# Optimization experiments

Measured on AMD Instinct MI355X. Metric: run time of the kernel, lower is better.

The kernel has to match this reference:

```python
import jax, jax.numpy as jnp
import numpy as np

B, S, D, H = 8, 2048, 1024, 8
HD = D // H


def _linear_params(key, d_in, d_out):
    kw, kb = jax.random.split(key)
    w = jax.random.normal(kw, (d_out, d_in), jnp.float32) * 0.02
    b = jax.random.normal(kb, (d_out,), jnp.float32) * 0.02
    return w, b


def setup_inputs() -> dict:
    key = jax.random.key(0)
    ks = jax.random.split(key, 16)
    inp = {}
    inp['input_seq'] = jax.random.normal(ks[0], (B, S, D), jnp.float32)
    inp['output_seq'] = jax.random.normal(ks[1], (B, S, D), jnp.float32)
    # PositionalEncoding parameter: sin(arange(D) / 10000 ** (arange(D)/D))
    ar = jnp.arange(D, dtype=jnp.float32)
    inp['pe'] = jnp.sin(ar / 10000.0 ** (ar / D))
    names = ['enc_wq enc_bq', 'enc_wk enc_bk', 'enc_wv enc_bv',
             'enc_w1 enc_b1', 'enc_w2 enc_b2',
             'dec_s_wq dec_s_bq', 'dec_s_wk dec_s_bk', 'dec_s_wv dec_s_bv',
             'dec_c_wq dec_c_bq', 'dec_c_wk dec_c_bk', 'dec_c_wv dec_c_bv',
             'dec_w1 dec_b1', 'dec_w2 dec_b2', 'fc_w fc_b']
    for i, pair in enumerate(names):
        wn, bn = pair.split()
        w, b = _linear_params(ks[2 + i], D, D)
        inp[wn], inp[bn] = w, b
    return inp


def _mha(q_in, k_in, wq, bq, wk, bk, wv, bv):
    # Faithful to source: head split WITHOUT transpose -> per-position 8x8 head mixing.
    q = (q_in @ wq.T + bq).reshape(q_in.shape[0], q_in.shape[1], H, HD)
    k = (k_in @ wk.T + bk).reshape(k_in.shape[0], k_in.shape[1], H, HD)
    v = (k_in @ wv.T + bv).reshape(k_in.shape[0], k_in.shape[1], H, HD)
    scores = jnp.einsum('bsih,bsjh->bsij', q, k) / jnp.sqrt(jnp.float32(HD))
    w = jax.nn.softmax(scores, axis=-1)  # dropout before softmax is identity at eval
    out = jnp.einsum('bsij,bsjh->bsih', w, v)
    return out.reshape(q_in.shape[0], q_in.shape[1], -1)


def reference(input_seq, output_seq, pe,
              enc_wq, enc_bq, enc_wk, enc_bk, enc_wv, enc_bv,
              enc_w1, enc_b1, enc_w2, enc_b2,
              dec_s_wq, dec_s_bq, dec_s_wk, dec_s_bk, dec_s_wv, dec_s_bv,
              dec_c_wq, dec_c_bq, dec_c_wk, dec_c_bk, dec_c_wv, dec_c_bv,
              dec_w1, dec_b1, dec_w2, dec_b2, fc_w, fc_b):
    x = input_seq + pe  # additive positional encoding
    # encoder layer
    a = _mha(x, x, enc_wq, enc_bq, enc_wk, enc_bk, enc_wv, enc_bv)
    enc_out = jax.nn.relu(a @ enc_w1.T + enc_b1) @ enc_w2.T + enc_b2
    # decoder layer (training branch: output_seq given)
    sa = _mha(output_seq, output_seq, dec_s_wq, dec_s_bq, dec_s_wk, dec_s_bk, dec_s_wv, dec_s_bv)
    ca = _mha(sa, enc_out, dec_c_wq, dec_c_bq, dec_c_wk, dec_c_bk, dec_c_wv, dec_c_bv)
    dec_out = jax.nn.relu(ca @ dec_w1.T + dec_b1) @ dec_w2.T + dec_b2
    return dec_out @ fc_w.T + fc_b
```

## Files before the change

### kernel.cpp

```cpp
#include <hip/hip_runtime.h>
#include <stdint.h>


#define TOKENS 16384
#define DMODEL 1024

typedef unsigned short ushort_t;
typedef __attribute__((ext_vector_type(8))) short short8;
typedef __attribute__((ext_vector_type(4))) float floatx4;

__device__ __forceinline__ float b2f(ushort_t u) {
  union { uint32_t i; float f; } v; v.i = ((uint32_t)u) << 16; return v.f;
}
__device__ __forceinline__ ushort_t f2b(float f) {
  union { float f; uint32_t i; } v; v.f = f;
  uint32_t r = v.i + 0x7fffu + ((v.i >> 16) & 1u);
  return (ushort_t)(r >> 16);
}

__device__ __forceinline__ void pack8(const float* __restrict__ g, ushort_t* dst) {
  float4 x = *(const float4*)g;
  float4 y = *(const float4*)(g + 4);
  ushort_t o[8] = {f2b(x.x), f2b(x.y), f2b(x.z), f2b(x.w),
                   f2b(y.x), f2b(y.y), f2b(y.z), f2b(y.w)};
  *(uint4*)dst = *(uint4*)o;
}

#define GLD16(g, l)                                                          \
  __builtin_amdgcn_global_load_lds(                                          \
      (const __attribute__((address_space(1))) void*)(g),                    \
      (__attribute__((address_space(3))) void*)(l), 16, 0, 0)

struct ConvArgs {
  const float* src[14];
  ushort_t* dst[14];
};

__global__ __launch_bounds__(256) void conv_w_kernel(ConvArgs a) {
  const int w = blockIdx.y;
  const int idx = (blockIdx.x * 256 + threadIdx.x) * 8;
  pack8(a.src[w] + idx, a.dst[w] + idx);
}

__global__ __launch_bounds__(256) void conv_x_kernel(
    const float* __restrict__ src, ushort_t* __restrict__ dst) {
  const int idx = (blockIdx.x * 256 + threadIdx.x) * 8;
  pack8(src + idx, dst + idx);
}

__global__ __launch_bounds__(256) void add_pe_kernel(
    const float* __restrict__ in, const float* __restrict__ pe,
    ushort_t* __restrict__ out) {
  int idx = (blockIdx.x * 256 + threadIdx.x) * 8;
  int d = idx & (DMODEL - 1);
  float4 a0 = *(const float4*)(in + idx);
  float4 a1 = *(const float4*)(in + idx + 4);
  float4 p0 = *(const float4*)(pe + d);
  float4 p1 = *(const float4*)(pe + d + 4);
  ushort_t o[8] = {f2b(a0.x + p0.x), f2b(a0.y + p0.y), f2b(a0.z + p0.z), f2b(a0.w + p0.w),
                   f2b(a1.x + p1.x), f2b(a1.y + p1.y), f2b(a1.z + p1.z), f2b(a1.w + p1.w)};
  *(uint4*)(out + idx) = *(uint4*)o;
}

template <int D, int MH>
__device__ __forceinline__ void load_a(const ushort_t* sA, int aoff, int cs0,
                                       int cs1, short8 (&af)[4][2]) {
  const ushort_t* p = sA + D * 16384 + MH * 8192 + aoff;
#pragma unroll
  for (int i = 0; i < 4; i++) {
    af[i][0] = *(const short8*)&p[i * 1024 + cs0];
    af[i][1] = *(const short8*)&p[i * 1024 + cs1];
  }
}

template <int D, int NH>
__device__ __forceinline__ void load_b(const ushort_t* sB, int boff, int cs0,
                                       int cs1, short8 (&bf)[2][2]) {
  const ushort_t* p = sB + D * 16384 + NH * 8192 + boff;
#pragma unroll
  for (int j = 0; j < 2; j++) {
    bf[j][0] = *(const short8*)&p[j * 1024 + cs0];
    bf[j][1] = *(const short8*)&p[j * 1024 + cs1];
  }
}

template <int Q>
__device__ __forceinline__ void mfma_q(floatx4 (&acc)[4][4][2],
                                       const short8 (&af)[4][2],
                                       const short8 (&bf)[2][2]) {
  __builtin_amdgcn_s_setprio(1);
#pragma unroll
  for (int i = 0; i < 4; i++)
#pragma unroll
    for (int j = 0; j < 2; j++) {
      acc[Q][i][j] = __builtin_amdgcn_mfma_f32_16x16x32_bf16(
          af[i][0], bf[j][0], acc[Q][i][j], 0, 0, 0);
      acc[Q][i][j] = __builtin_amdgcn_mfma_f32_16x16x32_bf16(
          af[i][1], bf[j][1], acc[Q][i][j], 0, 0, 0);
    }
  __builtin_amdgcn_s_setprio(0);
}

#define BARSB                                                                \
  do {                                                                       \
    __builtin_amdgcn_s_barrier();                                            \
    __builtin_amdgcn_sched_barrier(0);                                       \
  } while (0)

#define STAGE_A(h, tk, d)                                                    \
  do {                                                                       \
    GLD16(gA + (size_t)((h) * 131072 + (tk) * 64),                           \
          sA + (d) * 16384 + (h) * 8192 + lo);                               \
    GLD16(gA + (size_t)((h) * 131072 + 65536 + (tk) * 64),                   \
          sA + (d) * 16384 + (h) * 8192 + 4096 + lo);                        \
  } while (0)
#define STAGE_B(h, tk, d)                                                    \
  do {                                                                       \
    GLD16(gB + (size_t)((h) * 131072 + (tk) * 64),                           \
          sB + (d) * 16384 + (h) * 8192 + lo);                               \
    GLD16(gB + (size_t)((h) * 131072 + 65536 + (tk) * 64),                   \
          sB + (d) * 16384 + (h) * 8192 + 4096 + lo);                        \
  } while (0)

#define GROUP(tt, dd)                                                        \
  do {                                                                       \
    load_a<dd, 0>(sA, aoff, cs0, cs1, af);                                   \
    load_b<dd, 0>(sB, boff, cs0, cs1, bf);                                   \
    if ((tt) + 1 < NT) {                                                     \
      STAGE_B(0, (tt) + 1, dd ^ 1);                                          \
      STAGE_A(1, (tt) + 1, dd ^ 1);                                          \
    }                                                                        \
    BARSB;                                                                   \
    mfma_q<0>(acc, af, bf);                                                  \
    BARSB;                                                                   \
    load_b<dd, 1>(sB, boff, cs0, cs1, bf);                                   \
    BARSB;                                                                   \
    mfma_q<1>(acc, af, bf);                                                  \
    BARSB;                                                                   \
    load_a<dd, 1>(sA, aoff, cs0, cs1, af);                                   \
    if ((tt) + 2 < NT) STAGE_A(0, (tt) + 2, dd);                             \
    BARSB;                                                                   \
    mfma_q<3>(acc, af, bf);                                                  \
    BARSB;                                                                   \
    load_b<dd, 0>(sB, boff, cs0, cs1, bf);                                   \
    if ((tt) + 2 < NT) STAGE_B(1, (tt) + 2, dd);                             \
    BARSB;                                                                   \
    mfma_q<2>(acc, af, bf);                                                  \
    if ((tt) + 2 < NT) {                                                     \
      asm volatile("s_waitcnt vmcnt(4)");                                    \
    } else {                                                                 \
      asm volatile("s_waitcnt vmcnt(0)");                                    \
    }                                                                        \
    BARSB;                                                                   \
  } while (0)

template <bool RELU, bool OUT32>
__global__ __launch_bounds__(512, 2) void gemm_bt(
    const ushort_t* __restrict__ A, const ushort_t* __restrict__ W,
    const float* __restrict__ bias, void* __restrict__ Cp) {
  constexpr int K = 1024, N = 1024, NT = 16;
  extern __shared__ ushort_t smem[];
  ushort_t* sA = smem;
  ushort_t* sB = smem + 32768;

  const int tid = threadIdx.x;
  const int lane = tid & 63;
  const int wid = tid >> 6;

  const int orig = blockIdx.x;
  const int swz = (orig & 7) * 32 + (orig >> 3);
  const int m0 = (swz >> 2) * 256;
  const int n0 = (swz & 3) * 256;

  const int qm = (wid >> 2) * 64;
  const int qn = (wid & 3) * 32;
  const int lr = lane & 15;
  const int lq = lane >> 4;
  const int xr = lane & 7;
  const int cs0 = (lq ^ xr) * 8;
  const int cs1 = ((4 + lq) ^ xr) * 8;
  const int aoff = (qm + lr) * 64;
  const int boff = (qn + lr) * 64;

  const int rl = tid >> 3;
  const int j8 = tid & 7;
  const int co = (j8 ^ (rl & 7)) * 8;
  const int lo = tid * 8;
  const ushort_t* gA = A + (size_t)(m0 + rl) * K + co;
  const ushort_t* gB = W + (size_t)(n0 + rl) * K + co;

  floatx4 acc[4][4][2] = {};
  short8 af[4][2], bf[2][2];

  STAGE_A(0, 0, 0);
  STAGE_B(1, 0, 0);
  STAGE_B(0, 0, 0);
  STAGE_A(1, 0, 0);
  STAGE_A(0, 1, 1);
  STAGE_B(1, 1, 1);
  asm volatile("s_waitcnt vmcnt(4)");
  BARSB;

#pragma unroll 1
  for (int t = 0; t < NT; t += 2) {
    GROUP(t, 0);
    GROUP(t + 1, 1);
  }

  const int rbase = lq * 4;

  if constexpr (OUT32) {
    float* sCf = (float*)smem;
#pragma unroll
    for (int p = 0; p < 4; p++) {
      if ((qm >> 6) == (p & 1)) {
#pragma unroll
        for (int Nh = 0; Nh < 2; Nh++)
#pragma unroll
          for (int j = 0; j < 2; j++) {
            const int col = Nh * 128 + qn + j * 16 + lr;
            const float bv = bias[n0 + col];
#pragma unroll
            for (int i = 0; i < 4; i++)
#pragma unroll
              for (int r = 0; r < 4; r++) {
                float v = acc[(p >> 1) * 2 + Nh][i][j][r] + bv;
                if (RELU) v = fmaxf(v, 0.0f);
                sCf[(i * 16 + rbase + r) * 260 + col] = v;
              }
          }
      }
      __syncthreads();
#pragma unroll
      for (int u = 0; u < 8; u++) {
        const int lin = u * 512 + tid;
        const int row = lin >> 6;
        const int c4 = (lin & 63) * 4;
        *(float4*)((float*)Cp + (size_t)(m0 + p * 64 + row) * N + n0 + c4) =
            *(const float4*)&sCf[row * 260 + c4];
      }
      __syncthreads();
    }
    return;
  }

  ushort_t* sC = smem;
#pragma unroll
  for (int p = 0; p < 2; p++) {
#pragma unroll
    for (int Nh = 0; Nh < 2; Nh++)
#pragma unroll
      for (int j = 0; j < 2; j++) {
        const int col = Nh * 128 + qn + j * 16 + lr;
        const float bv = bias[n0 + col];
#pragma unroll
        for (int i = 0; i < 4; i++)
#pragma unroll
          for (int r = 0; r < 4; r++) {
            float v = acc[p * 2 + Nh][i][j][r] + bv;
            if (RELU) v = fmaxf(v, 0.0f);
            sC[(qm + i * 16 + rbase + r) * 264 + col] = f2b(v);
          }
      }
    __syncthreads();
#pragma unroll
    for (int u = 0; u < 8; u++) {
      const int lin = u * 512 + tid;
      const int row = lin >> 5;
      const int c8 = (lin & 31) * 8;
      *(uint4*)((ushort_t*)Cp + (size_t)(m0 + p * 128 + row) * N + n0 + c8) =
          *(const uint4*)&sC[row * 264 + c8];
    }
    __syncthreads();
  }
}

__global__ __launch_bounds__(256) void attn_kernel(
    const ushort_t* Q, const ushort_t* Kp, const ushort_t* Vp, ushort_t* O) {
  __shared__ __align__(16) ushort_t sq[4][1024];
  __shared__ __align__(16) ushort_t sk[4][1024];
  __shared__ __align__(16) ushort_t sv[4][1024];
  __shared__ float sp[4][64];

  const int t = threadIdx.x;
  const int w = t >> 6;
  const int lane = t & 63;
  const size_t base = ((size_t)blockIdx.x * 4 + w) * 1024;

  ((uint4*)sq[w])[lane] = ((const uint4*)(Q + base))[lane];
  ((uint4*)sq[w])[lane + 64] = ((const uint4*)(Q + base))[lane + 64];
  ((uint4*)sk[w])[lane] = ((const uint4*)(Kp + base))[lane];
  ((uint4*)sk[w])[lane + 64] = ((const uint4*)(Kp + base))[lane + 64];
  ((uint4*)sv[w])[lane] = ((const uint4*)(Vp + base))[lane];
  ((uint4*)sv[w])[lane + 64] = ((const uint4*)(Vp + base))[lane + 64];
  __syncthreads();

  {
    const int i = lane >> 3, j = lane & 7;
    const ushort_t* qr = &sq[w][i * 128];
    const ushort_t* kr = &sk[w][j * 128];
    float s = 0.0f;
#pragma unroll 16
    for (int h = 0; h < 128; h++) s += b2f(qr[h]) * b2f(kr[h]);
    s *= 0.08838834764831845f;
    float m = s;
#pragma unroll
    for (int off = 1; off < 8; off <<= 1) m = fmaxf(m, __shfl_xor(m, off, 64));
    float e = __expf(s - m);
    float sum = e;
#pragma unroll
    for (int off = 1; off < 8; off <<= 1) sum += __shfl_xor(sum, off, 64);
    sp[w][lane] = e / sum;
  }
  __syncthreads();

  {
    const int i = lane >> 3;
    const int hb = (lane & 7) * 16;
    float p[8];
#pragma unroll
    for (int jj = 0; jj < 8; jj++) p[jj] = sp[w][i * 8 + jj];
    float o[16];
#pragma unroll
    for (int h = 0; h < 16; h++) {
      float acc = 0.0f;
#pragma unroll
      for (int jj = 0; jj < 8; jj++) acc += p[jj] * b2f(sv[w][jj * 128 + hb + h]);
      o[h] = acc;
    }
    uint32_t packed[8];
#pragma unroll
    for (int u = 0; u < 8; u++)
      packed[u] = (uint32_t)f2b(o[2 * u]) | ((uint32_t)f2b(o[2 * u + 1]) << 16);
    uint4* dst = (uint4*)(O + base + i * 128 + hb);
    dst[0] = *(uint4*)&packed[0];
    dst[1] = *(uint4*)&packed[4];
  }
}

extern "C" void kernel_launch(void* const* d_in, const int* in_sizes, int n_in,
                              void* d_out, int out_size, void* d_ws, size_t ws_size,
                              hipStream_t stream) {
  const float* input_seq = (const float*)d_in[0];
  const float* output_seq = (const float*)d_in[1];
  const float* pe = (const float*)d_in[2];
  const float* wsrc[14] = {
      (const float*)d_in[3],  (const float*)d_in[5],  (const float*)d_in[7],
      (const float*)d_in[9],  (const float*)d_in[11], (const float*)d_in[13],
      (const float*)d_in[15], (const float*)d_in[17], (const float*)d_in[19],
      (const float*)d_in[21], (const float*)d_in[23], (const float*)d_in[25],
      (const float*)d_in[27], (const float*)d_in[29]};
  const float* enc_bq = (const float*)d_in[4];
  const float* enc_bk = (const float*)d_in[6];
  const float* enc_bv = (const float*)d_in[8];
  const float* enc_b1 = (const float*)d_in[10];
  const float* enc_b2 = (const float*)d_in[12];
  const float* dsq_b = (const float*)d_in[14];
  const float* dsk_b = (const float*)d_in[16];
  const float* dsv_b = (const float*)d_in[18];
  const float* dcq_b = (const float*)d_in[20];
  const float* dck_b = (const float*)d_in[22];
  const float* dcv_b = (const float*)d_in[24];
  const float* dec_b1 = (const float*)d_in[26];
  const float* dec_b2 = (const float*)d_in[28];
  const float* fc_b = (const float*)d_in[30];

  const size_t SZ = (size_t)TOKENS * DMODEL;
  const size_t WSZ = (size_t)DMODEL * DMODEL;
  ushort_t* bA = (ushort_t*)d_ws;
  ushort_t* bB = bA + SZ;
  ushort_t* oseq = bB + SZ;
  ushort_t* wts = oseq + SZ;
  ushort_t* oL = (ushort_t*)d_out;
  ushort_t* oH = oL + SZ;
  float* outf = (float*)d_out;

  static bool attr_set = false;
  if (!attr_set) {
    (void)hipFuncSetAttribute(reinterpret_cast<const void*>(&gemm_bt<false, false>),
                              hipFuncAttributeMaxDynamicSharedMemorySize, 131072);
    (void)hipFuncSetAttribute(reinterpret_cast<const void*>(&gemm_bt<true, false>),
                              hipFuncAttributeMaxDynamicSharedMemorySize, 131072);
    (void)hipFuncSetAttribute(reinterpret_cast<const void*>(&gemm_bt<false, true>),
                              hipFuncAttributeMaxDynamicSharedMemorySize, 131072);
    attr_set = true;
  }

  ConvArgs ca;
#pragma unroll
  for (int i = 0; i < 14; i++) { ca.src[i] = wsrc[i]; ca.dst[i] = wts + (size_t)i * WSZ; }

  const dim3 gG(TOKENS / 256 * (DMODEL / 256));
  const dim3 gblk(512);
  const dim3 blk(256);
  const int LDSB = 131072;
  const int gPE = TOKENS * DMODEL / (256 * 8);
  const int gAT = TOKENS / 4;

  conv_w_kernel<<<dim3(WSZ / (256 * 8), 14), blk, 0, stream>>>(ca);
  conv_x_kernel<<<gPE, blk, 0, stream>>>(output_seq, oseq);
  add_pe_kernel<<<gPE, blk, 0, stream>>>(input_seq, pe, bA);
  gemm_bt<false, false><<<gG, gblk, LDSB, stream>>>(bA, wts + 0 * WSZ, enc_bq, bB);
  gemm_bt<false, false><<<gG, gblk, LDSB, stream>>>(bA, wts + 1 * WSZ, enc_bk, oL);
  gemm_bt<false, false><<<gG, gblk, LDSB, stream>>>(bA, wts + 2 * WSZ, enc_bv, oH);
  attn_kernel<<<gAT, blk, 0, stream>>>(bB, oL, oH, bB);
  gemm_bt<true, false><<<gG, gblk, LDSB, stream>>>(bB, wts + 3 * WSZ, enc_b1, bA);
  gemm_bt<false, false><<<gG, gblk, LDSB, stream>>>(bA, wts + 4 * WSZ, enc_b2, bB);
  gemm_bt<false, false><<<gG, gblk, LDSB, stream>>>(oseq, wts + 5 * WSZ, dsq_b, bA);
  gemm_bt<false, false><<<gG, gblk, LDSB, stream>>>(oseq, wts + 6 * WSZ, dsk_b, oL);
  gemm_bt<false, false><<<gG, gblk, LDSB, stream>>>(oseq, wts + 7 * WSZ, dsv_b, oH);
  attn_kernel<<<gAT, blk, 0, stream>>>(bA, oL, oH, bA);
  gemm_bt<false, false><<<gG, gblk, LDSB, stream>>>(bA, wts + 8 * WSZ, dcq_b, oL);
  gemm_bt<false, false><<<gG, gblk, LDSB, stream>>>(bB, wts + 9 * WSZ, dck_b, oH);
  gemm_bt<false, false><<<gG, gblk, LDSB, stream>>>(bB, wts + 10 * WSZ, dcv_b, bA);
  attn_kernel<<<gAT, blk, 0, stream>>>(oL, oH, bA, oL);
  gemm_bt<true, false><<<gG, gblk, LDSB, stream>>>(oL, wts + 11 * WSZ, dec_b1, bB);
  gemm_bt<false, false><<<gG, gblk, LDSB, stream>>>(bB, wts + 12 * WSZ, dec_b2, bA);
  gemm_bt<false, true><<<gG, gblk, LDSB, stream>>>(bA, wts + 13 * WSZ, fc_b, outf);
}
```

Before: 832.3 us.

## Merge GEMM inner phases into two MFMA regions with fewer barriers

Restructures the GEMM main loop from four barrier-separated MFMA quarters into two larger regions. Both B fragments are loaded up front into separate registers, and each region runs two accumulator quadrants back to back. Block barriers per K-tile drop from eight to two, with explicit lgkmcnt waits before each barrier. The trade is higher register pressure from the extra B fragment set, which may threaten the 2-blocks-per-CU launch bound, and less interleaving of LDS reads with MFMA.

```diff
diff --git a/kernel.cpp b/kernel.cpp
--- a/kernel.cpp
+++ b/kernel.cpp
@@ -84,25 +84,36 @@
   }
 }
 
-template <int Q>
-__device__ __forceinline__ void mfma_q(floatx4 (&acc)[4][4][2],
-                                       const short8 (&af)[4][2],
-                                       const short8 (&bf)[2][2]) {
+template <int QA, int QB>
+__device__ __forceinline__ void mfma_region(floatx4 (&acc)[4][4][2],
+                                            const short8 (&af)[4][2],
+                                            const short8 (&b0)[2][2],
+                                            const short8 (&b1)[2][2]) {
   __builtin_amdgcn_s_setprio(1);
 #pragma unroll
   for (int i = 0; i < 4; i++)
 #pragma unroll
     for (int j = 0; j < 2; j++) {
-      acc[Q][i][j] = __builtin_amdgcn_mfma_f32_16x16x32_bf16(
-          af[i][0], bf[j][0], acc[Q][i][j], 0, 0, 0);
-      acc[Q][i][j] = __builtin_amdgcn_mfma_f32_16x16x32_bf16(
-          af[i][1], bf[j][1], acc[Q][i][j], 0, 0, 0);
+      acc[QA][i][j] = __builtin_amdgcn_mfma_f32_16x16x32_bf16(
+          af[i][0], b0[j][0], acc[QA][i][j], 0, 0, 0);
+      acc[QA][i][j] = __builtin_amdgcn_mfma_f32_16x16x32_bf16(
+          af[i][1], b0[j][1], acc[QA][i][j], 0, 0, 0);
+    }
+#pragma unroll
+  for (int i = 0; i < 4; i++)
+#pragma unroll
+    for (int j = 0; j < 2; j++) {
+      acc[QB][i][j] = __builtin_amdgcn_mfma_f32_16x16x32_bf16(
+          af[i][0], b1[j][0], acc[QB][i][j], 0, 0, 0);
+      acc[QB][i][j] = __builtin_amdgcn_mfma_f32_16x16x32_bf16(
+          af[i][1], b1[j][1], acc[QB][i][j], 0, 0, 0);
     }
   __builtin_amdgcn_s_setprio(0);
 }
 
-#define BARSB                                                                \
+#define BARRIER_PINNED                                                       \
   do {                                                                       \
+    __builtin_amdgcn_sched_barrier(0);                                       \
     __builtin_amdgcn_s_barrier();                                            \
     __builtin_amdgcn_sched_barrier(0);                                       \
   } while (0)
@@ -125,33 +136,28 @@
 #define GROUP(tt, dd)                                                        \
   do {                                                                       \
     load_a<dd, 0>(sA, aoff, cs0, cs1, af);                                   \
-    load_b<dd, 0>(sB, boff, cs0, cs1, bf);                                   \
+    load_b<dd, 0>(sB, boff, cs0, cs1, bf0);                                  \
+    load_b<dd, 1>(sB, boff, cs0, cs1, bf1);                                  \
     if ((tt) + 1 < NT) {                                                     \
-      STAGE_B(0, (tt) + 1, dd ^ 1);                                          \
-      STAGE_A(1, (tt) + 1, dd ^ 1);                                          \
+      STAGE_B(0, (tt) + 1, (dd) ^ 1);                                        \
+      STAGE_A(1, (tt) + 1, (dd) ^ 1);                                        \
     }                                                                        \
-    BARSB;                                                                   \
-    mfma_q<0>(acc, af, bf);                                                  \
-    BARSB;                                                                   \
-    load_b<dd, 1>(sB, boff, cs0, cs1, bf);                                   \
-    BARSB;                                                                   \
-    mfma_q<1>(acc, af, bf);                                                  \
-    BARSB;                                                                   \
+    mfma_region<0, 1>(acc, af, bf0, bf1);                                    \
+    asm volatile("s_waitcnt lgkmcnt(0)");                                    \
+    BARRIER_PINNED;                                                          \
     load_a<dd, 1>(sA, aoff, cs0, cs1, af);                                   \
-    if ((tt) + 2 < NT) STAGE_A(0, (tt) + 2, dd);                             \
-    BARSB;                                                                   \
-    mfma_q<3>(acc, af, bf);                                                  \
-    BARSB;                                                                   \
-    load_b<dd, 0>(sB, boff, cs0, cs1, bf);                                   \
-    if ((tt) + 2 < NT) STAGE_B(1, (tt) + 2, dd);                             \
-    BARSB;                                                                   \
-    mfma_q<2>(acc, af, bf);                                                  \
     if ((tt) + 2 < NT) {                                                     \
-      asm volatile("s_waitcnt vmcnt(4)");                                    \
-    } else {                                                                 \
-      asm volatile("s_waitcnt vmcnt(0)");                                    \
+      STAGE_A(0, (tt) + 2, dd);                                              \
+      STAGE_B(1, (tt) + 2, dd);                                              \
     }                                                                        \
-    BARSB;                                                                   \
+    mfma_region<2, 3>(acc, af, bf0, bf1);                                    \
+    if ((tt) + 2 < NT)                                                       \
+      asm volatile("s_waitcnt vmcnt(4) lgkmcnt(0)");                         \
+    else if ((tt) + 1 < NT)                                                  \
+      asm volatile("s_waitcnt vmcnt(0) lgkmcnt(0)");                         \
+    else                                                                     \
+      asm volatile("s_waitcnt lgkmcnt(0)");                                  \
+    BARRIER_PINNED;                                                          \
   } while (0)
 
 template <bool RELU, bool OUT32>
@@ -190,7 +196,7 @@
   const ushort_t* gB = W + (size_t)(n0 + rl) * K + co;
 
   floatx4 acc[4][4][2] = {};
-  short8 af[4][2], bf[2][2];
+  short8 af[4][2], bf0[2][2], bf1[2][2];
 
   STAGE_A(0, 0, 0);
   STAGE_B(1, 0, 0);
@@ -199,7 +205,7 @@
   STAGE_A(0, 1, 1);
   STAGE_B(1, 1, 1);
   asm volatile("s_waitcnt vmcnt(4)");
-  BARSB;
+  BARRIER_PINNED;
 
 #pragma unroll 1
   for (int t = 0; t < NT; t += 2) {
```

After: 822.9 us. Within noise of the previous version (-1.1%).
